# Kernel optimization log

Measured on AMD Instinct MI355X. Metric: run time of the kernel, lower is better.

Reference implementation:

```python
import jax, jax.numpy as jnp
from jax import lax
import numpy as np

P, L, T, DEG, D = 100000, 20000, 8, 48, 64  # n_paths, n_links, max_path_len, max_link_degree, state dim
ITERS = 4


def _relu(x):
    return jnp.maximum(x, 0.0)


def _gru_cell(x, h, wih, whh, bih, bhh):
    # PyTorch GRU gate math
    gi = x @ wih.T + bih
    gh = h @ whh.T + bhh
    ir, iz, inn = jnp.split(gi, 3, axis=-1)
    hr, hz, hn = jnp.split(gh, 3, axis=-1)
    r = jax.nn.sigmoid(ir + hr)
    z = jax.nn.sigmoid(iz + hz)
    n = jnp.tanh(inn + r * hn)
    return (1.0 - z) * n + z * h


def _forward(traffic, capacity, link_to_path, path_to_link,
             pe_w1, pe_b1, pe_w2, pe_b2,
             le_w1, le_b1, le_w2, le_b2,
             gru_wih, gru_whh, gru_bih, gru_bhh,
             cell_wih, cell_whh, cell_bih, cell_bhh,
             am_w1, am_b1, am_w2, am_b2, am_w3, am_b3):
    path_state = _relu(_relu(traffic @ pe_w1.T + pe_b1) @ pe_w2.T + pe_b2)   # [1,P,D]
    link_state = _relu(_relu(capacity @ le_w1.T + le_b1) @ le_w2.T + le_b2)  # [1,L,D]

    l2p = link_to_path[0]                      # [P,T]
    lmask = l2p != -1                          # [P,T]
    lengths = lmask.sum(axis=-1)               # [P]
    p2l = path_to_link[0]                      # [L,DEG,2]
    pmask = (p2l[..., 0] != -1)[..., None]     # [L,DEG,1]
    pidx = jnp.clip(p2l[..., 0], 0)
    posidx = jnp.clip(p2l[..., 1], 0)
    l2p_c = jnp.clip(l2p, 0)

    for _ in range(ITERS):
        # gather link states along each path, mask padding
        x = link_state[0][l2p_c] * lmask[..., None]        # [P,T,D]
        h0 = path_state[0]                                  # [P,D]

        def step(h, inp):
            xt, t = inp
            hn = _gru_cell(xt, h, gru_wih, gru_whh, gru_bih, gru_bhh)
            valid = (t < lengths)[:, None]
            h_new = jnp.where(valid, hn, h)          # packed-seq: hidden frozen past length
            out = jnp.where(valid, hn, 0.0)          # pad_packed: zeros past length
            return h_new, out

        h_final, outs = lax.scan(step, h0, (x.transpose(1, 0, 2), jnp.arange(T)))
        path_state = h_final[None]                          # [1,P,D]
        pss = jnp.concatenate([h0[:, None], outs.transpose(1, 0, 2)], axis=1)  # [P,T+1,D]

        gathered = pss[pidx, posidx] * pmask                # [L,DEG,D]
        pmin = jnp.where(pmask, gathered, jnp.inf).min(axis=-2)
        pmax = jnp.where(pmask, gathered, -jnp.inf).max(axis=-2)
        psum = jnp.where(pmask, gathered, 0.0).sum(axis=-2)
        cnt = jnp.maximum(pmask.sum(axis=-2), 1).astype(psum.dtype)
        pmean = psum / cnt
        agg = jnp.concatenate([pmin, pmax, psum, pmean], axis=-1)  # [L,4D]

        pa = _relu(_relu(_relu(agg @ am_w1.T + am_b1) @ am_w2.T + am_b2) @ am_w3.T + am_b3)
        link_state = _gru_cell(pa, link_state[0], cell_wih, cell_whh, cell_bih, cell_bhh)[None]

    return path_state, link_state


def setup_inputs() -> dict:
    key = jax.random.key(0)
    ks = jax.random.split(key, 40)
    w = lambda i, *s: jax.random.normal(ks[i], s, dtype=jnp.float32) * 0.1

    traffic = jax.random.uniform(ks[0], (1, P, 1), dtype=jnp.float32)
    capacity = jax.random.uniform(ks[1], (1, L, 1), dtype=jnp.float32)

    lengths = jax.random.randint(ks[2], (P,), 2, T + 1).at[0].set(T)
    lvalid = jnp.arange(T)[None, :] < lengths[:, None]
    link_to_path = jnp.where(lvalid, jax.random.randint(ks[3], (P, T), 0, L), -1)[None].astype(jnp.int32)

    deg = jax.random.randint(ks[4], (L,), 1, DEG + 1)
    dvalid = jnp.arange(DEG)[None, :] < deg[:, None]
    p0 = jnp.where(dvalid, jax.random.randint(ks[5], (L, DEG), 0, P), -1)
    p1 = jnp.where(dvalid, jax.random.randint(ks[6], (L, DEG), 0, T + 1), 0)
    path_to_link = jnp.stack([p0, p1], axis=-1)[None].astype(jnp.int32)

    return dict(
        traffic=traffic, capacity=capacity,
        link_to_path=link_to_path, path_to_link=path_to_link,
        pe_w1=w(10, D, 1), pe_b1=w(11, D), pe_w2=w(12, D, D), pe_b2=w(13, D),
        le_w1=w(14, D, 1), le_b1=w(15, D), le_w2=w(16, D, D), le_b2=w(17, D),
        gru_wih=w(18, 3 * D, D), gru_whh=w(19, 3 * D, D), gru_bih=w(20, 3 * D), gru_bhh=w(21, 3 * D),
        cell_wih=w(22, 3 * D, D), cell_whh=w(23, 3 * D, D), cell_bih=w(24, 3 * D), cell_bhh=w(25, 3 * D),
        am_w1=w(26, 2 * D, 4 * D), am_b1=w(27, 2 * D), am_w2=w(28, 2 * D, 2 * D), am_b2=w(29, 2 * D),
        am_w3=w(30, D, 2 * D), am_b3=w(31, D),
    )


def reference(traffic, capacity, link_to_path, path_to_link,
              pe_w1, pe_b1, pe_w2, pe_b2,
              le_w1, le_b1, le_w2, le_b2,
              gru_wih, gru_whh, gru_bih, gru_bhh,
              cell_wih, cell_whh, cell_bih, cell_bhh,
              am_w1, am_b1, am_w2, am_b2, am_w3, am_b3):
    return _forward(traffic, capacity, link_to_path, path_to_link,
                    pe_w1, pe_b1, pe_w2, pe_b2,
                    le_w1, le_b1, le_w2, le_b2,
                    gru_wih, gru_whh, gru_bih, gru_bhh,
                    cell_wih, cell_whh, cell_bih, cell_bhh,
                    am_w1, am_b1, am_w2, am_b2, am_w3, am_b3)
```

## Files before the change

kernel.cpp:

```cpp
#include <hip/hip_runtime.h>

#define P_N 100000
#define L_N 20000
#define T_N 8
#define DEG_N 48
#define D_N 64

#define W_PE_W1    0
#define W_PE_B1    64
#define W_PE_W2    128
#define W_PE_B2    4224
#define W_LE_W1    4288
#define W_LE_B1    4352
#define W_LE_W2    4416
#define W_LE_B2    8512
#define W_GRU_WIH  8576
#define W_GRU_WHH  20864
#define W_GRU_BIH  33152
#define W_GRU_BHH  33344
#define W_CELL_WIH 33536
#define W_CELL_WHH 45824
#define W_CELL_BIH 58112
#define W_CELL_BHH 58304
#define W_AM_W1    58496
#define W_AM_B1    91264
#define W_AM_W2    91392
#define W_AM_B2    107776
#define W_AM_W3    107904
#define W_AM_B3    116096
#define OFF_PS     116160
#define OFF_LS     (OFF_PS + P_N*D_N)
#define OFF_AG     (OFF_LS + L_N*D_N)
#define OFF_PSS    (OFF_AG + L_N*4*D_N)
#define PSS_U32    (P_N*9*D_N/2)
#define OFF_FLAG   (OFF_PSS + PSS_U32)
#define OFF_WIH16  (OFF_FLAG + 8)
#define OFF_WHH16  (OFF_WIH16 + 6144)
#define OFF_LS16   (OFF_WHH16 + 6144)
#define OFF_LW16   (OFF_LS16 + 640000)
#define OFF_LSLO   (OFF_LW16 + 81920)

typedef __attribute__((ext_vector_type(8))) short bf8_t;
typedef __attribute__((ext_vector_type(4))) float f4_t;
#define MFMA16(a,b,c) __builtin_amdgcn_mfma_f32_16x16x32_bf16(a,b,c,0,0,0)
#define LWLO 81920

__device__ __forceinline__ float bf2f(unsigned short u) {
    return __uint_as_float(((unsigned)u) << 16);
}
__device__ __forceinline__ unsigned short f2bf(float f) {
    unsigned u = __float_as_uint(f);
    unsigned r = u + 0x7FFFu + ((u >> 16) & 1u);
    return (unsigned short)(r >> 16);
}
__device__ __forceinline__ unsigned pk2(float a, float b) {
    return (unsigned)f2bf(a) | ((unsigned)f2bf(b) << 16);
}
__device__ __forceinline__ float fast_sig(float a) {
    return __builtin_amdgcn_rcpf(1.0f + __expf(-a));
}
__device__ __forceinline__ float fast_tanh(float a) {
    float s = __builtin_amdgcn_rcpf(1.0f + __expf(-2.0f * a));
    return fmaf(2.0f, s, -1.0f);
}
__device__ __forceinline__ void lds_barrier() {
    asm volatile("s_waitcnt lgkmcnt(0)" ::: "memory");
    __builtin_amdgcn_s_barrier();
    __builtin_amdgcn_sched_barrier(0);
}

__global__ void detect_k(const unsigned short* __restrict__ traffic, int* __restrict__ flag) {
    if (threadIdx.x == 0 && blockIdx.x == 0) {
        int plausible = 0;
        for (int i = 0; i < 64; ++i) {
            unsigned short v = traffic[i];
            int ex = (v >> 7) & 0xFF;
            if (!(v & 0x8000) && ex >= 0x6F && ex <= 0x7E) plausible++;
        }
        *flag = (plausible >= 56) ? 1 : 0;
    }
}

struct WSrc { const void* p[22]; };

__global__ void conv_weights_k(WSrc src, float* __restrict__ dst, const int* __restrict__ flag) {
    const int sz[22]  = {64,64,4096,64, 64,64,4096,64, 12288,12288,192,192,
                         12288,12288,192,192, 32768,128,16384,128,8192,64};
    const int off[22] = {0,64,128,4224, 4288,4352,4416,8512, 8576,20864,33152,33344,
                         33536,45824,58112,58304, 58496,91264,91392,107776,107904,116096};
    int a = blockIdx.x;
    float* d = dst + off[a];
    int n = sz[a];
    if (*flag) {
        const unsigned short* s = (const unsigned short*)src.p[a];
        for (int i = threadIdx.x; i < n; i += blockDim.x) d[i] = bf2f(s[i]);
    } else {
        const float* s = (const float*)src.p[a];
        for (int i = threadIdx.x; i < n; i += blockDim.x) d[i] = s[i];
    }
}

__global__ void conv_gru16_k(const float* __restrict__ ws,
                             unsigned short* __restrict__ wih, unsigned short* __restrict__ whh) {
    int i = blockIdx.x * 256 + threadIdx.x;
    if (i < 12288) { wih[i] = f2bf(ws[W_GRU_WIH + i]); whh[i] = f2bf(ws[W_GRU_WHH + i]); }
}

__global__ void conv_link16_k(const float* __restrict__ ws, unsigned short* __restrict__ lw) {
    int i = blockIdx.x * 256 + threadIdx.x;
    if (i >= 81920) return;
    float v;
    if (i < 32768)      v = ws[W_AM_W1 + i];
    else if (i < 49152) v = ws[W_AM_W2 + (i - 32768)];
    else if (i < 57344) v = ws[W_AM_W3 + (i - 49152)];
    else if (i < 69632) v = ws[W_CELL_WIH + (i - 57344)];
    else                v = ws[W_CELL_WHH + (i - 69632)];
    unsigned short hi = f2bf(v);
    lw[i] = hi;
    lw[LWLO + i] = f2bf(v - bf2f(hi));
}

__global__ void ls_to16_k(const float* __restrict__ ls, unsigned short* __restrict__ ohi,
                          unsigned short* __restrict__ olo) {
    int i = blockIdx.x * 256 + threadIdx.x;
    if (i < L_N * D_N) {
        float v = ls[i];
        unsigned short hi = f2bf(v);
        ohi[i] = hi;
        olo[i] = f2bf(v - bf2f(hi));
    }
}

__global__ __launch_bounds__(256) void embed_k(
    const void* __restrict__ inp,
    const float* __restrict__ w1, const float* __restrict__ b1,
    const float* __restrict__ w2, const float* __restrict__ b2,
    float* __restrict__ out, int N, const int* __restrict__ flag)
{
    int p = blockIdx.x * 256 + threadIdx.x;
    if (p >= N) return;
    float t = (*flag) ? bf2f(((const unsigned short*)inp)[p]) : ((const float*)inp)[p];
    float h1[64];
#pragma unroll
    for (int k = 0; k < 64; ++k) h1[k] = fmaxf(fmaf(t, w1[k], b1[k]), 0.0f);
#pragma unroll 1
    for (int j = 0; j < 64; ++j) {
        float acc = b2[j];
#pragma unroll
        for (int k = 0; k < 64; ++k) acc = fmaf(h1[k], w2[j * 64 + k], acc);
        out[p * 64 + j] = fmaxf(acc, 0.0f);
    }
}

__global__ __launch_bounds__(256, 3) void path_gru_mfma_k(
    const unsigned short* __restrict__ wih16,
    const unsigned short* __restrict__ whh16,
    const float* __restrict__ bih, const float* __restrict__ bhh,
    const unsigned short* __restrict__ ls16,
    float* __restrict__ path_state,
    const int* __restrict__ l2p, unsigned short* __restrict__ pss, int first)
{
    __shared__ __align__(16) unsigned short xt[2][32 * 72];
    __shared__ __align__(16) unsigned short ht[2][32 * 72];
    __shared__ int lint[32][8];
    __shared__ int lmaskA[32];

    const int tid = threadIdx.x;
    const int w = tid >> 6;
    const int L = tid & 63;
    const int col = L & 15;
    const int quad = L >> 4;
    const int p0 = blockIdx.x * 32;
    const int gpath = tid >> 4;
    const int gseg = tid & 15;

    if (tid < 32) {
        const int4* r4 = (const int4*)(l2p + (p0 + tid) * 8);
        int4 a = r4[0], b = r4[1];
        lint[tid][0] = a.x; lint[tid][1] = a.y; lint[tid][2] = a.z; lint[tid][3] = a.w;
        lint[tid][4] = b.x; lint[tid][5] = b.y; lint[tid][6] = b.z; lint[tid][7] = b.w;
        lmaskA[tid] = (a.x >= 0) | ((a.y >= 0) << 1) | ((a.z >= 0) << 2) | ((a.w >= 0) << 3)
                    | ((b.x >= 0) << 4) | ((b.y >= 0) << 5) | ((b.z >= 0) << 6) | ((b.w >= 0) << 7);
    }

    bf8_t BIr[2], BHr[2], BIz[2], BHz[2], BIn[2], BHn[2];
#pragma unroll
    for (int f = 0; f < 2; ++f) {
        int orr = ((w) * 16 + col) * 64 + f * 32 + quad * 8;
        int oz  = ((4 + w) * 16 + col) * 64 + f * 32 + quad * 8;
        int on  = ((8 + w) * 16 + col) * 64 + f * 32 + quad * 8;
        BIr[f] = *(const bf8_t*)(wih16 + orr);  BHr[f] = *(const bf8_t*)(whh16 + orr);
        BIz[f] = *(const bf8_t*)(wih16 + oz);   BHz[f] = *(const bf8_t*)(whh16 + oz);
        BIn[f] = *(const bf8_t*)(wih16 + on);   BHn[f] = *(const bf8_t*)(whh16 + on);
    }
    const float bR  = bih[w * 16 + col] + bhh[w * 16 + col];
    const float bZ  = bih[64 + w * 16 + col] + bhh[64 + w * 16 + col];
    const float bIN = bih[128 + w * 16 + col];
    const float bHN = bhh[128 + w * 16 + col];

    float hf[2][4];
#pragma unroll
    for (int pt = 0; pt < 2; ++pt)
#pragma unroll
        for (int r = 0; r < 4; ++r) {
            hf[pt][r] = path_state[(size_t)(p0 + pt * 16 + quad * 4 + r) * 64 + w * 16 + col];
            ht[0][(pt * 16 + quad * 4 + r) * 72 + w * 16 + col] = f2bf(hf[pt][r]);
        }

    lds_barrier();

    unsigned pm[2][4];
#pragma unroll
    for (int pt = 0; pt < 2; ++pt)
#pragma unroll
        for (int r = 0; r < 4; ++r) pm[pt][r] = (unsigned)lmaskA[pt * 16 + quad * 4 + r];
    const unsigned gm0 = (unsigned)lmaskA[gpath];
    const unsigned gm1 = (unsigned)lmaskA[gpath + 16];

#pragma unroll
    for (int h2 = 0; h2 < 2; ++h2) {
        const int gp = gpath + h2 * 16;
        int li = lint[gp][0];
        uint2 v; v.x = 0u; v.y = 0u;
        if (li >= 0) v = *(const uint2*)(ls16 + (size_t)li * 64 + gseg * 4);
        *(uint2*)(&xt[0][gp * 72 + gseg * 4]) = v;
    }
    lds_barrier();

#pragma unroll 2
    for (int t = 0; t < T_N; ++t) {
        const int cur = t & 1, nxt = (t + 1) & 1;

        uint2 pf[2];
#pragma unroll
        for (int h2 = 0; h2 < 2; ++h2) {
            const int gp = gpath + h2 * 16;
            const unsigned gm = h2 ? gm1 : gm0;
            uint2 hv = *(const uint2*)(&ht[cur][gp * 72 + gseg * 4]);
            int keep = (t == 0) ? 1 : (int)((gm >> (t - 1)) & 1);
            if (keep | first) {
                if (!keep) { hv.x = 0u; hv.y = 0u; }
                *(uint2*)(pss + (size_t)(p0 + gp) * 576 + t * 64 + gseg * 4) = hv;
            }
            pf[h2].x = 0u; pf[h2].y = 0u;
            if (t < T_N - 1) {
                int li = lint[gp][t + 1];
                if (li >= 0) pf[h2] = *(const uint2*)(ls16 + (size_t)li * 64 + gseg * 4);
            }
        }

#pragma unroll
        for (int pt = 0; pt < 2; ++pt) {
            bf8_t xA0 = *(const bf8_t*)(&xt[cur][(pt * 16 + col) * 72 + quad * 8]);
            bf8_t xA1 = *(const bf8_t*)(&xt[cur][(pt * 16 + col) * 72 + 32 + quad * 8]);
            bf8_t hA0 = *(const bf8_t*)(&ht[cur][(pt * 16 + col) * 72 + quad * 8]);
            bf8_t hA1 = *(const bf8_t*)(&ht[cur][(pt * 16 + col) * 72 + 32 + quad * 8]);

            f4_t aR = {bR, bR, bR, bR};
            f4_t aZ = {bZ, bZ, bZ, bZ};
            f4_t aI = {bIN, bIN, bIN, bIN};
            f4_t aH = {bHN, bHN, bHN, bHN};
            aR = MFMA16(xA0, BIr[0], aR); aR = MFMA16(xA1, BIr[1], aR);
            aR = MFMA16(hA0, BHr[0], aR); aR = MFMA16(hA1, BHr[1], aR);
            aZ = MFMA16(xA0, BIz[0], aZ); aZ = MFMA16(xA1, BIz[1], aZ);
            aZ = MFMA16(hA0, BHz[0], aZ); aZ = MFMA16(hA1, BHz[1], aZ);
            aI = MFMA16(xA0, BIn[0], aI); aI = MFMA16(xA1, BIn[1], aI);
            aH = MFMA16(hA0, BHn[0], aH); aH = MFMA16(hA1, BHn[1], aH);

#pragma unroll
            for (int r = 0; r < 4; ++r) {
                float rr = fast_sig(aR[r]);
                float zz = fast_sig(aZ[r]);
                float nn = fast_tanh(fmaf(rr, aH[r], aI[r]));
                float hb = hf[pt][r];
                float hv = fmaf(zz, hb - nn, nn);
                hf[pt][r] = ((pm[pt][r] >> t) & 1) ? hv : hb;
            }
#pragma unroll
            for (int r = 0; r < 4; ++r)
                ht[nxt][(pt * 16 + quad * 4 + r) * 72 + w * 16 + col] = f2bf(hf[pt][r]);
        }

        if (t < T_N - 1) {
#pragma unroll
            for (int h2 = 0; h2 < 2; ++h2)
                *(uint2*)(&xt[nxt][(gpath + h2 * 16) * 72 + gseg * 4]) = pf[h2];
        }
        lds_barrier();
    }

#pragma unroll
    for (int h2 = 0; h2 < 2; ++h2) {
        const int gp = gpath + h2 * 16;
        const unsigned gm = h2 ? gm1 : gm0;
        uint2 hv = *(const uint2*)(&ht[0][gp * 72 + gseg * 4]);
        int keep = (int)((gm >> 7) & 1);
        if (keep | first) {
            if (!keep) { hv.x = 0u; hv.y = 0u; }
            *(uint2*)(pss + (size_t)(p0 + gp) * 576 + 8 * 64 + gseg * 4) = hv;
        }
    }
#pragma unroll
    for (int pt = 0; pt < 2; ++pt)
#pragma unroll
        for (int r = 0; r < 4; ++r)
            path_state[(size_t)(p0 + pt * 16 + quad * 4 + r) * 64 + w * 16 + col] = hf[pt][r];
}

__global__ __launch_bounds__(256, 4) void link_agg_k(
    const int* __restrict__ p2l, const unsigned short* __restrict__ pss,
    unsigned short* __restrict__ agg16)
{
    const int lane = threadIdx.x & 63;
    const int l = __builtin_amdgcn_readfirstlane(blockIdx.x * 4 + (threadIdx.x >> 6));
    const int* __restrict__ row = p2l + (size_t)l * 96;

    float vmin = INFINITY, vmax = -INFINITY, vsum = 0.0f;
    int cnt = 0;
#pragma unroll
    for (int d = 0; d < DEG_N; ++d) {
        int pid = row[d * 2];
        int pos = row[d * 2 + 1];
        size_t off = (size_t)max(pid, 0) * 576 + (size_t)pos * 64 + lane;
        float v = bf2f(pss[off]);
        bool ok = pid >= 0;
        vmin = fminf(vmin, ok ? v : INFINITY);
        vmax = fmaxf(vmax, ok ? v : -INFINITY);
        vsum += ok ? v : 0.0f;
        cnt += ok ? 1 : 0;
    }
    float mean = vsum / (float)max(cnt, 1);

    unsigned short* rw = agg16 + (size_t)l * 512;
    float vals[4] = {vmin, vmax, vsum, mean};
#pragma unroll
    for (int c = 0; c < 4; ++c) {
        unsigned short hi = f2bf(vals[c]);
        rw[c * 64 + lane] = hi;
        rw[256 + c * 64 + lane] = f2bf(vals[c] - bf2f(hi));
    }
}

__global__ __launch_bounds__(64, 2) void link_upd_mfma_k(
    const unsigned short* __restrict__ lw,
    const float* __restrict__ b1, const float* __restrict__ b2, const float* __restrict__ b3,
    const float* __restrict__ cbih, const float* __restrict__ cbhh,
    const unsigned short* __restrict__ agg16,
    float* __restrict__ link_state,
    unsigned short* __restrict__ lshi, unsigned short* __restrict__ lslo)
{
    __shared__ __align__(16) unsigned short tile[2 * 16 * 136];
    const int L = threadIdx.x & 63;
    const int col = L & 15;
    const int quad = L >> 4;
    const int l0 = blockIdx.x * 16;
    const int mlink = min(l0 + col, L_N - 1);
    unsigned short* tlhi = &tile[0];
    unsigned short* tllo = &tile[16 * 136];

    const unsigned short* w1b = lw;
    const unsigned short* w2b = lw + 32768;
    const unsigned short* w3b = lw + 49152;
    const unsigned short* cih = lw + 57344;
    const unsigned short* chh = lw + 69632;

    {
        bf8_t Ah[8], Al[8];
#pragma unroll
        for (int f = 0; f < 8; ++f) {
            Ah[f] = *(const bf8_t*)(agg16 + (size_t)mlink * 512 + f * 32 + quad * 8);
            Al[f] = *(const bf8_t*)(agg16 + (size_t)mlink * 512 + 256 + f * 32 + quad * 8);
        }
#pragma unroll
        for (int nt = 0; nt < 8; ++nt) {
            float bb = b1[nt * 16 + col];
            f4_t acc = {bb, bb, bb, bb};
#pragma unroll
            for (int f = 0; f < 8; ++f) {
                size_t o = (size_t)(nt * 16 + col) * 256 + f * 32 + quad * 8;
                bf8_t Bh = *(const bf8_t*)(w1b + o);
                bf8_t Bl = *(const bf8_t*)(w1b + LWLO + o);
                acc = MFMA16(Ah[f], Bh, acc);
                acc = MFMA16(Ah[f], Bl, acc);
                acc = MFMA16(Al[f], Bh, acc);
            }
#pragma unroll
            for (int r = 0; r < 4; ++r) {
                float v = fmaxf(acc[r], 0.0f);
                unsigned short hi = f2bf(v);
                tlhi[(quad * 4 + r) * 136 + nt * 16 + col] = hi;
                tllo[(quad * 4 + r) * 136 + nt * 16 + col] = f2bf(v - bf2f(hi));
            }
        }
    }
    {
        bf8_t Ah[4], Al[4];
#pragma unroll
        for (int f = 0; f < 4; ++f) {
            Ah[f] = *(const bf8_t*)(tlhi + col * 136 + f * 32 + quad * 8);
            Al[f] = *(const bf8_t*)(tllo + col * 136 + f * 32 + quad * 8);
        }
        float vv[8][4];
#pragma unroll
        for (int nt = 0; nt < 8; ++nt) {
            float bb = b2[nt * 16 + col];
            f4_t acc = {bb, bb, bb, bb};
#pragma unroll
            for (int f = 0; f < 4; ++f) {
                size_t o = (size_t)(nt * 16 + col) * 128 + f * 32 + quad * 8;
                bf8_t Bh = *(const bf8_t*)(w2b + o);
                bf8_t Bl = *(const bf8_t*)(w2b + LWLO + o);
                acc = MFMA16(Ah[f], Bh, acc);
                acc = MFMA16(Ah[f], Bl, acc);
                acc = MFMA16(Al[f], Bh, acc);
            }
#pragma unroll
            for (int r = 0; r < 4; ++r) vv[nt][r] = fmaxf(acc[r], 0.0f);
        }
#pragma unroll
        for (int nt = 0; nt < 8; ++nt)
#pragma unroll
            for (int r = 0; r < 4; ++r) {
                unsigned short hi = f2bf(vv[nt][r]);
                tlhi[(quad * 4 + r) * 136 + nt * 16 + col] = hi;
                tllo[(quad * 4 + r) * 136 + nt * 16 + col] = f2bf(vv[nt][r] - bf2f(hi));
            }
    }
    {
        bf8_t Ah[4], Al[4];
#pragma unroll
        for (int f = 0; f < 4; ++f) {
            Ah[f] = *(const bf8_t*)(tlhi + col * 136 + f * 32 + quad * 8);
            Al[f] = *(const bf8_t*)(tllo + col * 136 + f * 32 + quad * 8);
        }
        float vv[4][4];
#pragma unroll
        for (int nt = 0; nt < 4; ++nt) {
            float bb = b3[nt * 16 + col];
            f4_t acc = {bb, bb, bb, bb};
#pragma unroll
            for (int f = 0; f < 4; ++f) {
                size_t o = (size_t)(nt * 16 + col) * 128 + f * 32 + quad * 8;
                bf8_t Bh = *(const bf8_t*)(w3b + o);
                bf8_t Bl = *(const bf8_t*)(w3b + LWLO + o);
                acc = MFMA16(Ah[f], Bh, acc);
                acc = MFMA16(Ah[f], Bl, acc);
                acc = MFMA16(Al[f], Bh, acc);
            }
#pragma unroll
            for (int r = 0; r < 4; ++r) vv[nt][r] = fmaxf(acc[r], 0.0f);
        }
#pragma unroll
        for (int nt = 0; nt < 4; ++nt)
#pragma unroll
            for (int r = 0; r < 4; ++r) {
                unsigned short hi = f2bf(vv[nt][r]);
                tlhi[(quad * 4 + r) * 136 + nt * 16 + col] = hi;
                tllo[(quad * 4 + r) * 136 + nt * 16 + col] = f2bf(vv[nt][r] - bf2f(hi));
            }
    }
    bf8_t xAh[2], xAl[2], hAh[2], hAl[2];
#pragma unroll
    for (int f = 0; f < 2; ++f) {
        xAh[f] = *(const bf8_t*)(tlhi + col * 136 + f * 32 + quad * 8);
        xAl[f] = *(const bf8_t*)(tllo + col * 136 + f * 32 + quad * 8);
        hAh[f] = *(const bf8_t*)(lshi + (size_t)mlink * 64 + f * 32 + quad * 8);
        hAl[f] = *(const bf8_t*)(lslo + (size_t)mlink * 64 + f * 32 + quad * 8);
    }
    float hf[16];
#pragma unroll
    for (int nt = 0; nt < 4; ++nt)
#pragma unroll
        for (int r = 0; r < 4; ++r) {
            int ml = min(l0 + quad * 4 + r, L_N - 1);
            hf[nt * 4 + r] = link_state[(size_t)ml * 64 + nt * 16 + col];
        }
    f4_t aRZ[8], aIN[4], aHN[4];
#pragma unroll
    for (int nt = 0; nt < 8; ++nt) {
        float bb = cbih[nt * 16 + col] + cbhh[nt * 16 + col];
        aRZ[nt][0] = bb; aRZ[nt][1] = bb; aRZ[nt][2] = bb; aRZ[nt][3] = bb;
    }
#pragma unroll
    for (int nt = 0; nt < 4; ++nt) {
        float bi = cbih[128 + nt * 16 + col], bh = cbhh[128 + nt * 16 + col];
        aIN[nt][0] = bi; aIN[nt][1] = bi; aIN[nt][2] = bi; aIN[nt][3] = bi;
        aHN[nt][0] = bh; aHN[nt][1] = bh; aHN[nt][2] = bh; aHN[nt][3] = bh;
    }
#pragma unroll
    for (int nt = 0; nt < 8; ++nt) {
#pragma unroll
        for (int f = 0; f < 2; ++f) {
            size_t o = (size_t)(nt * 16 + col) * 64 + f * 32 + quad * 8;
            bf8_t Bih = *(const bf8_t*)(cih + o);
            bf8_t Bil = *(const bf8_t*)(cih + LWLO + o);
            bf8_t Bhh = *(const bf8_t*)(chh + o);
            bf8_t Bhl = *(const bf8_t*)(chh + LWLO + o);
            aRZ[nt] = MFMA16(xAh[f], Bih, aRZ[nt]);
            aRZ[nt] = MFMA16(xAh[f], Bil, aRZ[nt]);
            aRZ[nt] = MFMA16(xAl[f], Bih, aRZ[nt]);
            aRZ[nt] = MFMA16(hAh[f], Bhh, aRZ[nt]);
            aRZ[nt] = MFMA16(hAh[f], Bhl, aRZ[nt]);
            aRZ[nt] = MFMA16(hAl[f], Bhh, aRZ[nt]);
        }
    }
#pragma unroll
    for (int nt = 0; nt < 4; ++nt) {
#pragma unroll
        for (int f = 0; f < 2; ++f) {
            size_t o = (size_t)((8 + nt) * 16 + col) * 64 + f * 32 + quad * 8;
            bf8_t Bih = *(const bf8_t*)(cih + o);
            bf8_t Bil = *(const bf8_t*)(cih + LWLO + o);
            bf8_t Bhh = *(const bf8_t*)(chh + o);
            bf8_t Bhl = *(const bf8_t*)(chh + LWLO + o);
            aIN[nt] = MFMA16(xAh[f], Bih, aIN[nt]);
            aIN[nt] = MFMA16(xAh[f], Bil, aIN[nt]);
            aIN[nt] = MFMA16(xAl[f], Bih, aIN[nt]);
            aHN[nt] = MFMA16(hAh[f], Bhh, aHN[nt]);
            aHN[nt] = MFMA16(hAh[f], Bhl, aHN[nt]);
            aHN[nt] = MFMA16(hAl[f], Bhh, aHN[nt]);
        }
    }
#pragma unroll
    for (int nt = 0; nt < 4; ++nt)
#pragma unroll
        for (int r = 0; r < 4; ++r) {
            int mrow = l0 + quad * 4 + r;
            float rr = fast_sig(aRZ[nt][r]);
            float zz = fast_sig(aRZ[nt + 4][r]);
            float nn = fast_tanh(fmaf(rr, aHN[nt][r], aIN[nt][r]));
            float hb = hf[nt * 4 + r];
            float hv = fmaf(zz, hb - nn, nn);
            if (mrow < L_N) {
                link_state[(size_t)mrow * 64 + nt * 16 + col] = hv;
                unsigned short hi = f2bf(hv);
                lshi[(size_t)mrow * 64 + nt * 16 + col] = hi;
                lslo[(size_t)mrow * 64 + nt * 16 + col] = f2bf(hv - bf2f(hi));
            }
        }
}

__global__ void final_out_k(const float* __restrict__ ps, const float* __restrict__ ls,
                            void* __restrict__ out, const int* __restrict__ flag)
{
    int i = blockIdx.x * 256 + threadIdx.x;
    int e = i * 2;
    float a, b;
    if (e < P_N * D_N) { a = ps[e]; b = ps[e + 1]; }
    else               { a = ls[e - P_N * D_N]; b = ls[e - P_N * D_N + 1]; }
    if (*flag) {
        ((unsigned*)out)[i] = pk2(a, b);
    } else {
        float2 v; v.x = a; v.y = b;
        ((float2*)out)[i] = v;
    }
}

extern "C" void kernel_launch(void* const* d_in, const int* in_sizes, int n_in,
                              void* d_out, int out_size, void* d_ws, size_t ws_size,
                              hipStream_t stream)
{
    const int* l2p = (const int*)d_in[2];
    const int* p2l = (const int*)d_in[3];
    float* ws = (float*)d_ws;
    int* flag = (int*)(ws + OFF_FLAG);
    unsigned short* wih16 = (unsigned short*)(ws + OFF_WIH16);
    unsigned short* whh16 = (unsigned short*)(ws + OFF_WHH16);
    unsigned short* lshi  = (unsigned short*)(ws + OFF_LS16);
    unsigned short* lslo  = (unsigned short*)(ws + OFF_LSLO);
    unsigned short* lw16  = (unsigned short*)(ws + OFF_LW16);
    unsigned short* agg16 = (unsigned short*)(ws + OFF_AG);
    unsigned short* pss   = (unsigned short*)(ws + OFF_PSS);

    detect_k<<<1, 64, 0, stream>>>((const unsigned short*)d_in[0], flag);

    WSrc srcs;
    for (int i = 0; i < 22; ++i) srcs.p[i] = d_in[4 + i];
    conv_weights_k<<<22, 256, 0, stream>>>(srcs, ws, flag);
    conv_gru16_k<<<48, 256, 0, stream>>>(ws, wih16, whh16);
    conv_link16_k<<<320, 256, 0, stream>>>(ws, lw16);

    embed_k<<<(P_N + 255) / 256, 256, 0, stream>>>(d_in[0], ws + W_PE_W1, ws + W_PE_B1,
                                                   ws + W_PE_W2, ws + W_PE_B2, ws + OFF_PS, P_N, flag);
    embed_k<<<(L_N + 255) / 256, 256, 0, stream>>>(d_in[1], ws + W_LE_W1, ws + W_LE_B1,
                                                   ws + W_LE_W2, ws + W_LE_B2, ws + OFF_LS, L_N, flag);
    ls_to16_k<<<(L_N * D_N + 255) / 256, 256, 0, stream>>>(ws + OFF_LS, lshi, lslo);

    for (int it = 0; it < 4; ++it) {
        path_gru_mfma_k<<<P_N / 32, 256, 0, stream>>>(
            wih16, whh16, ws + W_GRU_BIH, ws + W_GRU_BHH,
            lshi, ws + OFF_PS, l2p, pss, it == 0 ? 1 : 0);
        link_agg_k<<<L_N / 4, 256, 0, stream>>>(p2l, pss, agg16);
        link_upd_mfma_k<<<L_N / 16, 64, 0, stream>>>(
            lw16, ws + W_AM_B1, ws + W_AM_B2, ws + W_AM_B3,
            ws + W_CELL_BIH, ws + W_CELL_BHH,
            agg16, ws + OFF_LS, lshi, lslo);
    }
    final_out_k<<<(P_N * D_N + L_N * D_N) / 512, 256, 0, stream>>>(
        ws + OFF_PS, ws + OFF_LS, d_out, flag);
}
```

Measured before the change: 886.2 us.

## Double paths per GRU block and fuse bf16 conversion kernels

The path GRU kernel now handles 64 paths per block instead of 32, so each block loads the GRU weight fragments into registers once for twice as many paths. Per-path masks are packed into fewer registers, and bounds guards cover the partial final block. Separately, the two weight-conversion kernels are merged into one, and the link-state hi/lo bf16 split is folded into the link embedding kernel, removing two launches. The larger tile raises register and LDS pressure per block, which may reduce occupancy under the launch-bounds hint of 3.

```diff
diff --git a/kernel.cpp b/kernel.cpp
--- a/kernel.cpp
+++ b/kernel.cpp
@@ -100,34 +100,25 @@
     }
 }
 
-__global__ void conv_gru16_k(const float* __restrict__ ws,
-                             unsigned short* __restrict__ wih, unsigned short* __restrict__ whh) {
-    int i = blockIdx.x * 256 + threadIdx.x;
-    if (i < 12288) { wih[i] = f2bf(ws[W_GRU_WIH + i]); whh[i] = f2bf(ws[W_GRU_WHH + i]); }
-}
-
-__global__ void conv_link16_k(const float* __restrict__ ws, unsigned short* __restrict__ lw) {
-    int i = blockIdx.x * 256 + threadIdx.x;
-    if (i >= 81920) return;
-    float v;
-    if (i < 32768)      v = ws[W_AM_W1 + i];
-    else if (i < 49152) v = ws[W_AM_W2 + (i - 32768)];
-    else if (i < 57344) v = ws[W_AM_W3 + (i - 49152)];
-    else if (i < 69632) v = ws[W_CELL_WIH + (i - 57344)];
-    else                v = ws[W_CELL_WHH + (i - 69632)];
-    unsigned short hi = f2bf(v);
-    lw[i] = hi;
-    lw[LWLO + i] = f2bf(v - bf2f(hi));
-}
-
-__global__ void ls_to16_k(const float* __restrict__ ls, unsigned short* __restrict__ ohi,
-                          unsigned short* __restrict__ olo) {
-    int i = blockIdx.x * 256 + threadIdx.x;
-    if (i < L_N * D_N) {
-        float v = ls[i];
+__global__ void conv_bf16_k(const float* __restrict__ ws,
+                            unsigned short* __restrict__ wih, unsigned short* __restrict__ whh,
+                            unsigned short* __restrict__ lw) {
+    int b = blockIdx.x;
+    if (b < 48) {
+        int i = b * 256 + threadIdx.x;
+        if (i < 12288) { wih[i] = f2bf(ws[W_GRU_WIH + i]); whh[i] = f2bf(ws[W_GRU_WHH + i]); }
+    } else {
+        int i = (b - 48) * 256 + threadIdx.x;
+        if (i >= 81920) return;
+        float v;
+        if (i < 32768)      v = ws[W_AM_W1 + i];
+        else if (i < 49152) v = ws[W_AM_W2 + (i - 32768)];
+        else if (i < 57344) v = ws[W_AM_W3 + (i - 49152)];
+        else if (i < 69632) v = ws[W_CELL_WIH + (i - 57344)];
+        else                v = ws[W_CELL_WHH + (i - 69632)];
         unsigned short hi = f2bf(v);
-        ohi[i] = hi;
-        olo[i] = f2bf(v - bf2f(hi));
+        lw[i] = hi;
+        lw[LWLO + i] = f2bf(v - bf2f(hi));
     }
 }
 
@@ -135,7 +126,8 @@
     const void* __restrict__ inp,
     const float* __restrict__ w1, const float* __restrict__ b1,
     const float* __restrict__ w2, const float* __restrict__ b2,
-    float* __restrict__ out, int N, const int* __restrict__ flag)
+    float* __restrict__ out, unsigned short* __restrict__ ohi,
+    unsigned short* __restrict__ olo, int N, const int* __restrict__ flag)
 {
     int p = blockIdx.x * 256 + threadIdx.x;
     if (p >= N) return;
@@ -148,7 +140,13 @@
         float acc = b2[j];
 #pragma unroll
         for (int k = 0; k < 64; ++k) acc = fmaf(h1[k], w2[j * 64 + k], acc);
-        out[p * 64 + j] = fmaxf(acc, 0.0f);
+        float v = fmaxf(acc, 0.0f);
+        out[p * 64 + j] = v;
+        if (ohi) {
+            unsigned short hi = f2bf(v);
+            ohi[p * 64 + j] = hi;
+            olo[p * 64 + j] = f2bf(v - bf2f(hi));
+        }
     }
 }
 
@@ -160,22 +158,22 @@
     float* __restrict__ path_state,
     const int* __restrict__ l2p, unsigned short* __restrict__ pss, int first)
 {
-    __shared__ __align__(16) unsigned short xt[2][32 * 72];
-    __shared__ __align__(16) unsigned short ht[2][32 * 72];
-    __shared__ int lint[32][8];
-    __shared__ int lmaskA[32];
+    __shared__ __align__(16) unsigned short xt[2][64 * 72];
+    __shared__ __align__(16) unsigned short ht[2][64 * 72];
+    __shared__ int lint[64][8];
+    __shared__ int lmaskA[64];
 
     const int tid = threadIdx.x;
     const int w = tid >> 6;
     const int L = tid & 63;
     const int col = L & 15;
     const int quad = L >> 4;
-    const int p0 = blockIdx.x * 32;
+    const int p0 = blockIdx.x * 64;
     const int gpath = tid >> 4;
     const int gseg = tid & 15;
 
-    if (tid < 32) {
-        const int4* r4 = (const int4*)(l2p + (p0 + tid) * 8);
+    if (tid < 64) {
+        const int4* r4 = (const int4*)(l2p + (size_t)min(p0 + tid, P_N - 1) * 8);
         int4 a = r4[0], b = r4[1];
         lint[tid][0] = a.x; lint[tid][1] = a.y; lint[tid][2] = a.z; lint[tid][3] = a.w;
         lint[tid][4] = b.x; lint[tid][5] = b.y; lint[tid][6] = b.z; lint[tid][7] = b.w;
@@ -198,27 +196,32 @@
     const float bIN = bih[128 + w * 16 + col];
     const float bHN = bhh[128 + w * 16 + col];
 
-    float hf[2][4];
-#pragma unroll
-    for (int pt = 0; pt < 2; ++pt)
+    float hf[4][4];
+#pragma unroll
+    for (int pt = 0; pt < 4; ++pt)
 #pragma unroll
         for (int r = 0; r < 4; ++r) {
-            hf[pt][r] = path_state[(size_t)(p0 + pt * 16 + quad * 4 + r) * 64 + w * 16 + col];
+            hf[pt][r] = path_state[(size_t)min(p0 + pt * 16 + quad * 4 + r, P_N - 1) * 64
+                                   + w * 16 + col];
             ht[0][(pt * 16 + quad * 4 + r) * 72 + w * 16 + col] = f2bf(hf[pt][r]);
         }
 
     lds_barrier();
 
-    unsigned pm[2][4];
-#pragma unroll
-    for (int pt = 0; pt < 2; ++pt)
-#pragma unroll
-        for (int r = 0; r < 4; ++r) pm[pt][r] = (unsigned)lmaskA[pt * 16 + quad * 4 + r];
-    const unsigned gm0 = (unsigned)lmaskA[gpath];
-    const unsigned gm1 = (unsigned)lmaskA[gpath + 16];
-
-#pragma unroll
-    for (int h2 = 0; h2 < 2; ++h2) {
+    unsigned pmp[4];
+#pragma unroll
+    for (int pt = 0; pt < 4; ++pt)
+        pmp[pt] = (unsigned)lmaskA[pt * 16 + quad * 4 + 0]
+                | ((unsigned)lmaskA[pt * 16 + quad * 4 + 1] << 8)
+                | ((unsigned)lmaskA[pt * 16 + quad * 4 + 2] << 16)
+                | ((unsigned)lmaskA[pt * 16 + quad * 4 + 3] << 24);
+    const unsigned gmp = (unsigned)lmaskA[gpath]
+                       | ((unsigned)lmaskA[gpath + 16] << 8)
+                       | ((unsigned)lmaskA[gpath + 32] << 16)
+                       | ((unsigned)lmaskA[gpath + 48] << 24);
+
+#pragma unroll
+    for (int h2 = 0; h2 < 4; ++h2) {
         const int gp = gpath + h2 * 16;
         int li = lint[gp][0];
         uint2 v; v.x = 0u; v.y = 0u;
@@ -231,14 +234,13 @@
     for (int t = 0; t < T_N; ++t) {
         const int cur = t & 1, nxt = (t + 1) & 1;
 
-        uint2 pf[2];
-#pragma unroll
-        for (int h2 = 0; h2 < 2; ++h2) {
+        uint2 pf[4];
+#pragma unroll
+        for (int h2 = 0; h2 < 4; ++h2) {
             const int gp = gpath + h2 * 16;
-            const unsigned gm = h2 ? gm1 : gm0;
             uint2 hv = *(const uint2*)(&ht[cur][gp * 72 + gseg * 4]);
-            int keep = (t == 0) ? 1 : (int)((gm >> (t - 1)) & 1);
-            if (keep | first) {
+            int keep = (t == 0) ? 1 : (int)((gmp >> (h2 * 8 + t - 1)) & 1);
+            if ((keep | first) && (p0 + gp) < P_N) {
                 if (!keep) { hv.x = 0u; hv.y = 0u; }
                 *(uint2*)(pss + (size_t)(p0 + gp) * 576 + t * 64 + gseg * 4) = hv;
             }
@@ -250,7 +252,7 @@
         }
 
 #pragma unroll
-        for (int pt = 0; pt < 2; ++pt) {
+        for (int pt = 0; pt < 4; ++pt) {
             bf8_t xA0 = *(const bf8_t*)(&xt[cur][(pt * 16 + col) * 72 + quad * 8]);
             bf8_t xA1 = *(const bf8_t*)(&xt[cur][(pt * 16 + col) * 72 + 32 + quad * 8]);
             bf8_t hA0 = *(const bf8_t*)(&ht[cur][(pt * 16 + col) * 72 + quad * 8]);
@@ -274,7 +276,7 @@
                 float nn = fast_tanh(fmaf(rr, aH[r], aI[r]));
                 float hb = hf[pt][r];
                 float hv = fmaf(zz, hb - nn, nn);
-                hf[pt][r] = ((pm[pt][r] >> t) & 1) ? hv : hb;
+                hf[pt][r] = ((pmp[pt] >> (r * 8 + t)) & 1) ? hv : hb;
             }
 #pragma unroll
             for (int r = 0; r < 4; ++r)
@@ -283,28 +285,30 @@
 
         if (t < T_N - 1) {
 #pragma unroll
-            for (int h2 = 0; h2 < 2; ++h2)
+            for (int h2 = 0; h2 < 4; ++h2)
                 *(uint2*)(&xt[nxt][(gpath + h2 * 16) * 72 + gseg * 4]) = pf[h2];
         }
         lds_barrier();
     }
 
 #pragma unroll
-    for (int h2 = 0; h2 < 2; ++h2) {
+    for (int h2 = 0; h2 < 4; ++h2) {
         const int gp = gpath + h2 * 16;
-        const unsigned gm = h2 ? gm1 : gm0;
         uint2 hv = *(const uint2*)(&ht[0][gp * 72 + gseg * 4]);
-        int keep = (int)((gm >> 7) & 1);
-        if (keep | first) {
+        int keep = (int)((gmp >> (h2 * 8 + 7)) & 1);
+        if ((keep | first) && (p0 + gp) < P_N) {
             if (!keep) { hv.x = 0u; hv.y = 0u; }
             *(uint2*)(pss + (size_t)(p0 + gp) * 576 + 8 * 64 + gseg * 4) = hv;
         }
     }
 #pragma unroll
-    for (int pt = 0; pt < 2; ++pt)
-#pragma unroll
-        for (int r = 0; r < 4; ++r)
-            path_state[(size_t)(p0 + pt * 16 + quad * 4 + r) * 64 + w * 16 + col] = hf[pt][r];
+    for (int pt = 0; pt < 4; ++pt)
+#pragma unroll
+        for (int r = 0; r < 4; ++r) {
+            int prow = p0 + pt * 16 + quad * 4 + r;
+            if (prow < P_N)
+                path_state[(size_t)prow * 64 + w * 16 + col] = hf[pt][r];
+        }
 }
 
 __global__ __launch_bounds__(256, 4) void link_agg_k(
@@ -577,17 +581,18 @@
     WSrc srcs;
     for (int i = 0; i < 22; ++i) srcs.p[i] = d_in[4 + i];
     conv_weights_k<<<22, 256, 0, stream>>>(srcs, ws, flag);
-    conv_gru16_k<<<48, 256, 0, stream>>>(ws, wih16, whh16);
-    conv_link16_k<<<320, 256, 0, stream>>>(ws, lw16);
+    conv_bf16_k<<<368, 256, 0, stream>>>(ws, wih16, whh16, lw16);
 
     embed_k<<<(P_N + 255) / 256, 256, 0, stream>>>(d_in[0], ws + W_PE_W1, ws + W_PE_B1,
-                                                   ws + W_PE_W2, ws + W_PE_B2, ws + OFF_PS, P_N, flag);
+                                                   ws + W_PE_W2, ws + W_PE_B2, ws + OFF_PS,
+                                                   (unsigned short*)nullptr, (unsigned short*)nullptr,
+                                                   P_N, flag);
     embed_k<<<(L_N + 255) / 256, 256, 0, stream>>>(d_in[1], ws + W_LE_W1, ws + W_LE_B1,
-                                                   ws + W_LE_W2, ws + W_LE_B2, ws + OFF_LS, L_N, flag);
-    ls_to16_k<<<(L_N * D_N + 255) / 256, 256, 0, stream>>>(ws + OFF_LS, lshi, lslo);
+                                                   ws + W_LE_W2, ws + W_LE_B2, ws + OFF_LS,
+                                                   lshi, lslo, L_N, flag);
 
     for (int it = 0; it < 4; ++it) {
-        path_gru_mfma_k<<<P_N / 32, 256, 0, stream>>>(
+        path_gru_mfma_k<<<(P_N + 63) / 64, 256, 0, stream>>>(
             wih16, whh16, ws + W_GRU_BIH, ws + W_GRU_BHH,
             lshi, ws + OFF_PS, l2p, pss, it == 0 ? 1 : 0);
         link_agg_k<<<L_N / 4, 256, 0, stream>>>(p2l, pss, agg16);
```

After: 944.8 us. 1.07x slower.

## Fuse link aggregation into link update kernel and merge setup conversion kernels

Applied to the files above, without the earlier changes.

The per-link min/max/sum/mean gather now runs inside the link update kernel. Each 64-thread block aggregates its 16 links into shared memory before the MFMA MLP and GRU, instead of writing and re-reading an aggregate buffer in global memory. The weight conversion kernels are merged into one launch, and the bf16 hi/lo split of link state moves into the embedding kernel. This removes launches and a global round trip, but the gather now runs serially per block with far fewer waves in flight, which reduces latency hiding for the random loads.

```diff
diff --git a/kernel.cpp b/kernel.cpp
--- a/kernel.cpp
+++ b/kernel.cpp
@@ -100,34 +100,25 @@
     }
 }
 
-__global__ void conv_gru16_k(const float* __restrict__ ws,
-                             unsigned short* __restrict__ wih, unsigned short* __restrict__ whh) {
-    int i = blockIdx.x * 256 + threadIdx.x;
-    if (i < 12288) { wih[i] = f2bf(ws[W_GRU_WIH + i]); whh[i] = f2bf(ws[W_GRU_WHH + i]); }
-}
-
-__global__ void conv_link16_k(const float* __restrict__ ws, unsigned short* __restrict__ lw) {
-    int i = blockIdx.x * 256 + threadIdx.x;
-    if (i >= 81920) return;
-    float v;
-    if (i < 32768)      v = ws[W_AM_W1 + i];
-    else if (i < 49152) v = ws[W_AM_W2 + (i - 32768)];
-    else if (i < 57344) v = ws[W_AM_W3 + (i - 49152)];
-    else if (i < 69632) v = ws[W_CELL_WIH + (i - 57344)];
-    else                v = ws[W_CELL_WHH + (i - 69632)];
-    unsigned short hi = f2bf(v);
-    lw[i] = hi;
-    lw[LWLO + i] = f2bf(v - bf2f(hi));
-}
-
-__global__ void ls_to16_k(const float* __restrict__ ls, unsigned short* __restrict__ ohi,
-                          unsigned short* __restrict__ olo) {
-    int i = blockIdx.x * 256 + threadIdx.x;
-    if (i < L_N * D_N) {
-        float v = ls[i];
+__global__ void conv_bf16_k(const float* __restrict__ ws,
+                            unsigned short* __restrict__ wih, unsigned short* __restrict__ whh,
+                            unsigned short* __restrict__ lw) {
+    int b = blockIdx.x;
+    if (b < 48) {
+        int i = b * 256 + threadIdx.x;
+        if (i < 12288) { wih[i] = f2bf(ws[W_GRU_WIH + i]); whh[i] = f2bf(ws[W_GRU_WHH + i]); }
+    } else {
+        int i = (b - 48) * 256 + threadIdx.x;
+        if (i >= 81920) return;
+        float v;
+        if (i < 32768)      v = ws[W_AM_W1 + i];
+        else if (i < 49152) v = ws[W_AM_W2 + (i - 32768)];
+        else if (i < 57344) v = ws[W_AM_W3 + (i - 49152)];
+        else if (i < 69632) v = ws[W_CELL_WIH + (i - 57344)];
+        else                v = ws[W_CELL_WHH + (i - 69632)];
         unsigned short hi = f2bf(v);
-        ohi[i] = hi;
-        olo[i] = f2bf(v - bf2f(hi));
+        lw[i] = hi;
+        lw[LWLO + i] = f2bf(v - bf2f(hi));
     }
 }
 
@@ -135,7 +126,8 @@
     const void* __restrict__ inp,
     const float* __restrict__ w1, const float* __restrict__ b1,
     const float* __restrict__ w2, const float* __restrict__ b2,
-    float* __restrict__ out, int N, const int* __restrict__ flag)
+    float* __restrict__ out, unsigned short* __restrict__ ohi,
+    unsigned short* __restrict__ olo, int N, const int* __restrict__ flag)
 {
     int p = blockIdx.x * 256 + threadIdx.x;
     if (p >= N) return;
@@ -148,7 +140,13 @@
         float acc = b2[j];
 #pragma unroll
         for (int k = 0; k < 64; ++k) acc = fmaf(h1[k], w2[j * 64 + k], acc);
-        out[p * 64 + j] = fmaxf(acc, 0.0f);
+        float v = fmaxf(acc, 0.0f);
+        out[p * 64 + j] = v;
+        if (ohi) {
+            unsigned short hi = f2bf(v);
+            ohi[p * 64 + j] = hi;
+            olo[p * 64 + j] = f2bf(v - bf2f(hi));
+        }
     }
 }
 
@@ -307,54 +305,51 @@
             path_state[(size_t)(p0 + pt * 16 + quad * 4 + r) * 64 + w * 16 + col] = hf[pt][r];
 }
 
-__global__ __launch_bounds__(256, 4) void link_agg_k(
+__global__ __launch_bounds__(64, 2) void link_fused_k(
     const int* __restrict__ p2l, const unsigned short* __restrict__ pss,
-    unsigned short* __restrict__ agg16)
-{
-    const int lane = threadIdx.x & 63;
-    const int l = __builtin_amdgcn_readfirstlane(blockIdx.x * 4 + (threadIdx.x >> 6));
-    const int* __restrict__ row = p2l + (size_t)l * 96;
-
-    float vmin = INFINITY, vmax = -INFINITY, vsum = 0.0f;
-    int cnt = 0;
-#pragma unroll
-    for (int d = 0; d < DEG_N; ++d) {
-        int pid = row[d * 2];
-        int pos = row[d * 2 + 1];
-        size_t off = (size_t)max(pid, 0) * 576 + (size_t)pos * 64 + lane;
-        float v = bf2f(pss[off]);
-        bool ok = pid >= 0;
-        vmin = fminf(vmin, ok ? v : INFINITY);
-        vmax = fmaxf(vmax, ok ? v : -INFINITY);
-        vsum += ok ? v : 0.0f;
-        cnt += ok ? 1 : 0;
-    }
-    float mean = vsum / (float)max(cnt, 1);
-
-    unsigned short* rw = agg16 + (size_t)l * 512;
-    float vals[4] = {vmin, vmax, vsum, mean};
-#pragma unroll
-    for (int c = 0; c < 4; ++c) {
-        unsigned short hi = f2bf(vals[c]);
-        rw[c * 64 + lane] = hi;
-        rw[256 + c * 64 + lane] = f2bf(vals[c] - bf2f(hi));
-    }
-}
-
-__global__ __launch_bounds__(64, 2) void link_upd_mfma_k(
     const unsigned short* __restrict__ lw,
     const float* __restrict__ b1, const float* __restrict__ b2, const float* __restrict__ b3,
     const float* __restrict__ cbih, const float* __restrict__ cbhh,
-    const unsigned short* __restrict__ agg16,
     float* __restrict__ link_state,
     unsigned short* __restrict__ lshi, unsigned short* __restrict__ lslo)
 {
+    __shared__ __align__(16) unsigned short aggL[16 * 520];
     __shared__ __align__(16) unsigned short tile[2 * 16 * 136];
-    const int L = threadIdx.x & 63;
-    const int col = L & 15;
-    const int quad = L >> 4;
+    const int lane = threadIdx.x & 63;
+    const int col = lane & 15;
+    const int quad = lane >> 4;
     const int l0 = blockIdx.x * 16;
-    const int mlink = min(l0 + col, L_N - 1);
+
+#pragma unroll 1
+    for (int k = 0; k < 16; ++k) {
+        const int l = __builtin_amdgcn_readfirstlane(l0 + k);
+        const int* __restrict__ row = p2l + (size_t)l * 96;
+        float vmin = INFINITY, vmax = -INFINITY, vsum = 0.0f;
+        int cnt = 0;
+#pragma unroll
+        for (int d = 0; d < DEG_N; ++d) {
+            int pid = row[d * 2];
+            int pos = row[d * 2 + 1];
+            size_t off = (size_t)max(pid, 0) * 576 + (size_t)pos * 64 + lane;
+            float v = bf2f(pss[off]);
+            bool ok = pid >= 0;
+            vmin = fminf(vmin, ok ? v : INFINITY);
+            vmax = fmaxf(vmax, ok ? v : -INFINITY);
+            vsum += ok ? v : 0.0f;
+            cnt += ok ? 1 : 0;
+        }
+        float mean = vsum / (float)max(cnt, 1);
+        unsigned short* rw = aggL + k * 520;
+        float vals[4] = {vmin, vmax, vsum, mean};
+#pragma unroll
+        for (int c = 0; c < 4; ++c) {
+            unsigned short hi = f2bf(vals[c]);
+            rw[c * 64 + lane] = hi;
+            rw[256 + c * 64 + lane] = f2bf(vals[c] - bf2f(hi));
+        }
+    }
+
+    const int mlink = l0 + col;
     unsigned short* tlhi = &tile[0];
     unsigned short* tllo = &tile[16 * 136];
 
@@ -368,8 +363,8 @@
         bf8_t Ah[8], Al[8];
 #pragma unroll
         for (int f = 0; f < 8; ++f) {
-            Ah[f] = *(const bf8_t*)(agg16 + (size_t)mlink * 512 + f * 32 + quad * 8);
-            Al[f] = *(const bf8_t*)(agg16 + (size_t)mlink * 512 + 256 + f * 32 + quad * 8);
+            Ah[f] = *(const bf8_t*)(aggL + col * 520 + f * 32 + quad * 8);
+            Al[f] = *(const bf8_t*)(aggL + col * 520 + 256 + f * 32 + quad * 8);
         }
 #pragma unroll
         for (int nt = 0; nt < 8; ++nt) {
@@ -471,10 +466,8 @@
 #pragma unroll
     for (int nt = 0; nt < 4; ++nt)
 #pragma unroll
-        for (int r = 0; r < 4; ++r) {
-            int ml = min(l0 + quad * 4 + r, L_N - 1);
-            hf[nt * 4 + r] = link_state[(size_t)ml * 64 + nt * 16 + col];
-        }
+        for (int r = 0; r < 4; ++r)
+            hf[nt * 4 + r] = link_state[(size_t)(l0 + quad * 4 + r) * 64 + nt * 16 + col];
     f4_t aRZ[8], aIN[4], aHN[4];
 #pragma unroll
     for (int nt = 0; nt < 8; ++nt) {
@@ -531,12 +524,10 @@
             float nn = fast_tanh(fmaf(rr, aHN[nt][r], aIN[nt][r]));
             float hb = hf[nt * 4 + r];
             float hv = fmaf(zz, hb - nn, nn);
-            if (mrow < L_N) {
-                link_state[(size_t)mrow * 64 + nt * 16 + col] = hv;
-                unsigned short hi = f2bf(hv);
-                lshi[(size_t)mrow * 64 + nt * 16 + col] = hi;
-                lslo[(size_t)mrow * 64 + nt * 16 + col] = f2bf(hv - bf2f(hi));
-            }
+            link_state[(size_t)mrow * 64 + nt * 16 + col] = hv;
+            unsigned short hi = f2bf(hv);
+            lshi[(size_t)mrow * 64 + nt * 16 + col] = hi;
+            lslo[(size_t)mrow * 64 + nt * 16 + col] = f2bf(hv - bf2f(hi));
         }
 }
 
@@ -569,7 +560,6 @@
     unsigned short* lshi  = (unsigned short*)(ws + OFF_LS16);
     unsigned short* lslo  = (unsigned short*)(ws + OFF_LSLO);
     unsigned short* lw16  = (unsigned short*)(ws + OFF_LW16);
-    unsigned short* agg16 = (unsigned short*)(ws + OFF_AG);
     unsigned short* pss   = (unsigned short*)(ws + OFF_PSS);
 
     detect_k<<<1, 64, 0, stream>>>((const unsigned short*)d_in[0], flag);
@@ -577,24 +567,25 @@
     WSrc srcs;
     for (int i = 0; i < 22; ++i) srcs.p[i] = d_in[4 + i];
     conv_weights_k<<<22, 256, 0, stream>>>(srcs, ws, flag);
-    conv_gru16_k<<<48, 256, 0, stream>>>(ws, wih16, whh16);
-    conv_link16_k<<<320, 256, 0, stream>>>(ws, lw16);
+    conv_bf16_k<<<368, 256, 0, stream>>>(ws, wih16, whh16, lw16);
 
     embed_k<<<(P_N + 255) / 256, 256, 0, stream>>>(d_in[0], ws + W_PE_W1, ws + W_PE_B1,
-                                                   ws + W_PE_W2, ws + W_PE_B2, ws + OFF_PS, P_N, flag);
+                                                   ws + W_PE_W2, ws + W_PE_B2, ws + OFF_PS,
+                                                   (unsigned short*)nullptr, (unsigned short*)nullptr,
+                                                   P_N, flag);
     embed_k<<<(L_N + 255) / 256, 256, 0, stream>>>(d_in[1], ws + W_LE_W1, ws + W_LE_B1,
-                                                   ws + W_LE_W2, ws + W_LE_B2, ws + OFF_LS, L_N, flag);
-    ls_to16_k<<<(L_N * D_N + 255) / 256, 256, 0, stream>>>(ws + OFF_LS, lshi, lslo);
+                                                   ws + W_LE_W2, ws + W_LE_B2, ws + OFF_LS,
+                                                   lshi, lslo, L_N, flag);
 
     for (int it = 0; it < 4; ++it) {
         path_gru_mfma_k<<<P_N / 32, 256, 0, stream>>>(
             wih16, whh16, ws + W_GRU_BIH, ws + W_GRU_BHH,
             lshi, ws + OFF_PS, l2p, pss, it == 0 ? 1 : 0);
-        link_agg_k<<<L_N / 4, 256, 0, stream>>>(p2l, pss, agg16);
-        link_upd_mfma_k<<<L_N / 16, 64, 0, stream>>>(
-            lw16, ws + W_AM_B1, ws + W_AM_B2, ws + W_AM_B3,
+        link_fused_k<<<L_N / 16, 64, 0, stream>>>(
+            p2l, pss, lw16,
+            ws + W_AM_B1, ws + W_AM_B2, ws + W_AM_B3,
             ws + W_CELL_BIH, ws + W_CELL_BHH,
-            agg16, ws + OFF_LS, lshi, lslo);
+            ws + OFF_LS, lshi, lslo);
     }
     final_out_k<<<(P_N * D_N + L_N * D_N) / 512, 256, 0, stream>>>(
         ws + OFF_PS, ws + OFF_LS, d_out, flag);
```

Measured after the change: 1.269 ms. 43.2% more time.
